# Kernel optimization log

Hardware: AMD Instinct MI355X
Metric: run time of the kernel (lower is better)

The kernel has to match this reference:

```python
import jax, jax.numpy as jnp
import numpy as np

N, IN_SIZE, FEAT, N_OUT = 8192, 512, 128, 512
ALPHA = 0.5


def setup_inputs() -> dict:
    key = jax.random.key(0)
    ks = jax.random.split(key, 5)
    return {
        "x": jax.random.normal(ks[0], (N, IN_SIZE), dtype=jnp.float32),
        "W0": jax.random.normal(ks[1], (FEAT, IN_SIZE), dtype=jnp.float32) * (1.0 / np.sqrt(IN_SIZE)),
        "W1": jax.random.normal(ks[2], (FEAT, IN_SIZE), dtype=jnp.float32) * (1.0 / np.sqrt(IN_SIZE)),
        "weight": jax.random.normal(ks[3], (IN_SIZE, N_OUT), dtype=jnp.float32),
        "weight_time": jax.random.normal(ks[4], (IN_SIZE, N_OUT), dtype=jnp.float32),
    }


def time_affinity(n: int) -> jnp.ndarray:
    # Closed form of the numpy roll/triu/flip construction: M[i,j] = n - |i-j|,
    # then rows normalized to sum to 1.
    idx = jnp.arange(n)
    M = (n - jnp.abs(idx[:, None] - idx[None, :])).astype(jnp.float32)
    return M / jnp.sum(M, axis=1, keepdims=True)


def reference(x, W0, W1, weight, weight_time):
    n = x.shape[0]
    q = x @ W0.T                      # [N, FEAT]
    k = x @ W1.T                      # [N, FEAT]
    G = jax.nn.softmax(q @ k.T, axis=1)   # [N, N] learned affinity
    G_time = time_affinity(n)              # [N, N] static affinity
    out = (G @ x) @ weight                 # [N, N_OUT]
    out_time = (G_time @ x) @ weight_time  # [N, N_OUT]
    return ALPHA * out + (1.0 - ALPHA) * out_time
```

## Files before the change

kernel.cpp:

```cpp
#include <hip/hip_runtime.h>
#include <math.h>

#define NN 8192
#define INS 512
#define FEAT 128

typedef unsigned short ush;
typedef short bf16x8 __attribute__((ext_vector_type(8)));
typedef float f32x4 __attribute__((ext_vector_type(4)));

__device__ __forceinline__ ush f2bf(float f) {
    unsigned u = __float_as_uint(f);
    unsigned r = (u + 0x7FFFu + ((u >> 16) & 1u)) >> 16;
    return (ush)r;
}
__device__ __forceinline__ float bf2f(ush h) {
    return __uint_as_float(((unsigned)h) << 16);
}
__device__ __forceinline__ void cp16(const ush* g, ush* l) {
    __builtin_amdgcn_global_load_lds(
        (const __attribute__((address_space(1))) void*)g,
        (__attribute__((address_space(3))) void*)l, 16, 0, 0);
}
__device__ __forceinline__ void split8(float4 f0, float4 f1, uint4& h, uint4& l) {
    float f[8] = {f0.x, f0.y, f0.z, f0.w, f1.x, f1.y, f1.z, f1.w};
    unsigned hu[8], lu[8];
    #pragma unroll
    for (int j = 0; j < 8; ++j) {
        unsigned u = __float_as_uint(f[j]);
        hu[j] = u >> 16;
        float lo = f[j] - __uint_as_float(u & 0xFFFF0000u);
        lu[j] = (unsigned)f2bf(lo);
    }
    h.x = hu[0] | (hu[1] << 16); h.y = hu[2] | (hu[3] << 16);
    h.z = hu[4] | (hu[5] << 16); h.w = hu[6] | (hu[7] << 16);
    l.x = lu[0] | (lu[1] << 16); l.y = lu[2] | (lu[3] << 16);
    l.z = lu[4] | (lu[5] << 16); l.w = lu[6] | (lu[7] << 16);
}


__global__ __launch_bounds__(256) void cast_w01(const float* __restrict__ W0,
                                                const float* __restrict__ W1,
                                                ush* __restrict__ W01h,
                                                ush* __restrict__ W01l) {
    int idx = (blockIdx.x * 256 + threadIdx.x) * 8;
    int r = idx >> 9, c = idx & 511;
    const float* src = (r < 128) ? &W0[r * 512 + c] : &W1[(r - 128) * 512 + c];
    float4 f0 = *(const float4*)src;
    float4 f1 = *(const float4*)(src + 4);
    uint4 h, l;
    split8(f0, f1, h, l);
    *(uint4*)&W01h[idx] = h;
    *(uint4*)&W01l[idx] = l;
}

__global__ __launch_bounds__(256) void cast_wT(const float* __restrict__ wm,
                                               const float* __restrict__ wt,
                                               ush* __restrict__ wmTh, ush* __restrict__ wmTl,
                                               ush* __restrict__ wtTh, ush* __restrict__ wtTl) {
    const float* src = blockIdx.z ? wt : wm;
    ush* oh = blockIdx.z ? wtTh : wmTh;
    ush* ol = blockIdx.z ? wtTl : wmTl;
    __shared__ float T[64][65];
    const int t = threadIdx.x;
    const int k0 = blockIdx.y * 64, n0 = blockIdx.x * 64;
    #pragma unroll
    for (int u = 0; u < 4; ++u) {
        int idx = u * 256 + t;
        int r = idx >> 4, c4 = (idx & 15) * 4;
        *(float4*)&T[r][c4] = *(const float4*)&src[(k0 + r) * 512 + n0 + c4];
    }
    __syncthreads();
    #pragma unroll
    for (int u = 0; u < 4; ++u) {
        int idx = u * 256 + t;
        int a = idx >> 4, b4 = (idx & 15) * 4;
        unsigned hu[4], lu[4];
        #pragma unroll
        for (int j = 0; j < 4; ++j) {
            float f = T[b4 + j][a];
            unsigned uu = __float_as_uint(f);
            hu[j] = uu >> 16;
            lu[j] = (unsigned)f2bf(f - __uint_as_float(uu & 0xFFFF0000u));
        }
        uint2 hp, lp;
        hp.x = hu[0] | (hu[1] << 16); hp.y = hu[2] | (hu[3] << 16);
        lp.x = lu[0] | (lu[1] << 16); lp.y = lu[2] | (lu[3] << 16);
        *(uint2*)&oh[(n0 + a) * 512 + k0 + b4] = hp;
        *(uint2*)&ol[(n0 + a) * 512 + k0 + b4] = lp;
    }
}

__global__ __launch_bounds__(256) void gemm_xv(const float* __restrict__ x,
    const ush* __restrict__ wmTh, const ush* __restrict__ wmTl,
    const ush* __restrict__ wtTh, const ush* __restrict__ wtTl,
    ush* __restrict__ vtg, ush* __restrict__ xtb) {
    const bool isV = (blockIdx.z == 0);
    const ush* Bhg = isV ? wmTh : wtTh;
    const ush* Blg = isV ? wmTl : wtTl;
    __shared__ __align__(16) ush sm[20480];
    ush* Ah = sm;
    ush* Al = sm + 5120;
    ush* Bh = sm + 10240;
    ush* Bl = sm + 15360;
    const int t = threadIdx.x;
    const int lane = t & 63, w = t >> 6;
    const int l15 = lane & 15, g4 = lane >> 4;
    const int m0 = blockIdx.y * 128, n0 = blockIdx.x * 128;
    const int wm0 = (w & 1) * 64, wn0 = (w >> 1) * 64;
    f32x4 acc[4][4];
    #pragma unroll
    for (int mt = 0; mt < 4; ++mt)
        #pragma unroll
        for (int nt = 0; nt < 4; ++nt)
            acc[mt][nt] = (f32x4){0.f, 0.f, 0.f, 0.f};

    const int am = t >> 1, akh = (t & 1) * 16;
    for (int k0 = 0; k0 < 512; k0 += 32) {
        __syncthreads();
        {
            const float* src = &x[(m0 + am) * 512 + k0 + akh];
            float4 f0 = *(const float4*)&src[0];
            float4 f1 = *(const float4*)&src[4];
            float4 f2 = *(const float4*)&src[8];
            float4 f3 = *(const float4*)&src[12];
            uint4 h0, l0, h1, l1;
            split8(f0, f1, h0, l0);
            split8(f2, f3, h1, l1);
            int s0 = am * 5 + (akh >> 3);
            *(uint4*)&Ah[s0 * 8] = h0; *(uint4*)&Ah[(s0 + 1) * 8] = h1;
            *(uint4*)&Al[s0 * 8] = l0; *(uint4*)&Al[(s0 + 1) * 8] = l1;
        }
        #pragma unroll
        for (int u = 0; u < 2; ++u) {
            int s = u * 256 + t;
            int n = s >> 2, g = s & 3;
            int srco = (n0 + n) * 512 + k0 + g * 8;
            int slot = n * 5 + g;
            *(uint4*)&Bh[slot * 8] = *(const uint4*)&Bhg[srco];
            *(uint4*)&Bl[slot * 8] = *(const uint4*)&Blg[srco];
        }
        __syncthreads();
        bf16x8 ah[4], al[4], bh[4], bl[4];
        #pragma unroll
        for (int mt = 0; mt < 4; ++mt) {
            int slot = (wm0 + mt * 16 + l15) * 5 + g4;
            ah[mt] = *(const bf16x8*)&Ah[slot * 8];
            al[mt] = *(const bf16x8*)&Al[slot * 8];
        }
        #pragma unroll
        for (int nt = 0; nt < 4; ++nt) {
            int slot = (wn0 + nt * 16 + l15) * 5 + g4;
            bh[nt] = *(const bf16x8*)&Bh[slot * 8];
            bl[nt] = *(const bf16x8*)&Bl[slot * 8];
        }
        #pragma unroll
        for (int mt = 0; mt < 4; ++mt)
            #pragma unroll
            for (int nt = 0; nt < 4; ++nt) {
                acc[mt][nt] = __builtin_amdgcn_mfma_f32_16x16x32_bf16(ah[mt], bh[nt], acc[mt][nt], 0, 0, 0);
                acc[mt][nt] = __builtin_amdgcn_mfma_f32_16x16x32_bf16(al[mt], bh[nt], acc[mt][nt], 0, 0, 0);
                acc[mt][nt] = __builtin_amdgcn_mfma_f32_16x16x32_bf16(ah[mt], bl[nt], acc[mt][nt], 0, 0, 0);
            }
    }

    if (!isV) {
        #pragma unroll
        for (int mt = 0; mt < 4; ++mt)
            #pragma unroll
            for (int nt = 0; nt < 4; ++nt) {
                int col = n0 + wn0 + nt * 16 + l15;
                int rowb = m0 + wm0 + mt * 16 + g4 * 4;
                #pragma unroll
                for (int reg = 0; reg < 4; ++reg)
                    xtb[(rowb + reg) * 512 + col] = f2bf(acc[mt][nt][reg]);
            }
    } else {
        __syncthreads();
        #pragma unroll
        for (int mt = 0; mt < 4; ++mt)
            #pragma unroll
            for (int nt = 0; nt < 4; ++nt) {
                int nl = wn0 + nt * 16 + l15;
                int mb = wm0 + mt * 16 + g4 * 4;
                uint2 pk;
                pk.x = (unsigned)f2bf(acc[mt][nt][0]) | ((unsigned)f2bf(acc[mt][nt][1]) << 16);
                pk.y = (unsigned)f2bf(acc[mt][nt][2]) | ((unsigned)f2bf(acc[mt][nt][3]) << 16);
                *(uint2*)&sm[nl * 136 + mb] = pk;
            }
        __syncthreads();
        int a = t >> 1, off = (t & 1) * 64;
        #pragma unroll
        for (int u = 0; u < 8; ++u)
            *(uint4*)&vtg[(n0 + a) * 8192 + m0 + off + u * 8] =
                *(const uint4*)&sm[a * 136 + off + u * 8];
    }
}

__global__ __launch_bounds__(256) void gemm_qk(const float* __restrict__ x,
    const ush* __restrict__ W01h, const ush* __restrict__ W01l,
    ush* __restrict__ qh, ush* __restrict__ ql,
    ush* __restrict__ kh, ush* __restrict__ kl) {
    __shared__ __align__(16) ush sm[15360];
    ush* Ah = sm;
    ush* Al = sm + 2560;
    ush* Bh = sm + 5120;
    ush* Bl = sm + 10240;
    const int t = threadIdx.x;
    const int lane = t & 63, w = t >> 6;
    const int l15 = lane & 15, g4 = lane >> 4;
    const int m0 = blockIdx.y * 64, n0 = blockIdx.x * 128;
    const int wm0 = (w & 1) * 32, wn0 = (w >> 1) * 64;
    f32x4 acc[2][4];
    #pragma unroll
    for (int mt = 0; mt < 2; ++mt)
        #pragma unroll
        for (int nt = 0; nt < 4; ++nt)
            acc[mt][nt] = (f32x4){0.f, 0.f, 0.f, 0.f};

    const int ar = t >> 2, ag = t & 3;
    for (int k0 = 0; k0 < 512; k0 += 32) {
        __syncthreads();
        {
            const float* src = &x[(m0 + ar) * 512 + k0 + ag * 8];
            float4 f0 = *(const float4*)&src[0];
            float4 f1 = *(const float4*)&src[4];
            uint4 h, l;
            split8(f0, f1, h, l);
            int slot = ar * 5 + ag;
            *(uint4*)&Ah[slot * 8] = h;
            *(uint4*)&Al[slot * 8] = l;
        }
        #pragma unroll
        for (int u = 0; u < 2; ++u) {
            int s = u * 256 + t;
            int n = s >> 2, g = s & 3;
            int srco = (n0 + n) * 512 + k0 + g * 8;
            int slot = n * 5 + g;
            *(uint4*)&Bh[slot * 8] = *(const uint4*)&W01h[srco];
            *(uint4*)&Bl[slot * 8] = *(const uint4*)&W01l[srco];
        }
        __syncthreads();
        bf16x8 ah[2], al[2], bh[4], bl[4];
        #pragma unroll
        for (int mt = 0; mt < 2; ++mt) {
            int slot = (wm0 + mt * 16 + l15) * 5 + g4;
            ah[mt] = *(const bf16x8*)&Ah[slot * 8];
            al[mt] = *(const bf16x8*)&Al[slot * 8];
        }
        #pragma unroll
        for (int nt = 0; nt < 4; ++nt) {
            int slot = (wn0 + nt * 16 + l15) * 5 + g4;
            bh[nt] = *(const bf16x8*)&Bh[slot * 8];
            bl[nt] = *(const bf16x8*)&Bl[slot * 8];
        }
        #pragma unroll
        for (int mt = 0; mt < 2; ++mt)
            #pragma unroll
            for (int nt = 0; nt < 4; ++nt) {
                acc[mt][nt] = __builtin_amdgcn_mfma_f32_16x16x32_bf16(ah[mt], bh[nt], acc[mt][nt], 0, 0, 0);
                acc[mt][nt] = __builtin_amdgcn_mfma_f32_16x16x32_bf16(al[mt], bh[nt], acc[mt][nt], 0, 0, 0);
                acc[mt][nt] = __builtin_amdgcn_mfma_f32_16x16x32_bf16(ah[mt], bl[nt], acc[mt][nt], 0, 0, 0);
            }
    }
    ush* oh = (n0 == 0) ? qh : kh;
    ush* ol = (n0 == 0) ? ql : kl;
    #pragma unroll
    for (int mt = 0; mt < 2; ++mt)
        #pragma unroll
        for (int nt = 0; nt < 4; ++nt) {
            int col = wn0 + nt * 16 + l15;
            int rowb = m0 + wm0 + mt * 16 + g4 * 4;
            #pragma unroll
            for (int reg = 0; reg < 4; ++reg) {
                float v = acc[mt][nt][reg];
                unsigned u = __float_as_uint(v);
                ush h = (ush)(u >> 16);
                ush lo = f2bf(v - __uint_as_float(u & 0xFFFF0000u));
                oh[(rowb + reg) * 128 + col] = h;
                ol[(rowb + reg) * 128 + col] = lo;
            }
        }
}

__global__ __launch_bounds__(256) void time_part1(const ush* __restrict__ xtb,
                                                  float* __restrict__ pP,
                                                  float* __restrict__ pQ) {
    int d = blockIdx.x * 256 + threadIdx.x;
    int r0 = blockIdx.y * 128;
    float sp = 0.f, sq = 0.f;
    for (int r = 0; r < 128; ++r) {
        float v = bf2f(xtb[(r0 + r) * 512 + d]);
        sp += v;
        sq += (float)(r0 + r) * v;
    }
    pP[blockIdx.y * 512 + d] = sp;
    pQ[blockIdx.y * 512 + d] = sq;
}

__global__ __launch_bounds__(512) void time_part2(float* __restrict__ pP,
                                                  float* __restrict__ pQ,
                                                  float* __restrict__ Ad,
                                                  float* __restrict__ Qt) {
    int d = threadIdx.x;
    float rp = 0.f, rq = 0.f;
    for (int c = 0; c < 64; ++c) {
        int idx = c * 512 + d;
        float p = pP[idx], qv = pQ[idx];
        pP[idx] = rp; pQ[idx] = rq;
        rp += p; rq += qv;
    }
    Ad[d] = rp; Qt[d] = rq;
}

__global__ __launch_bounds__(256) void time_part3(const ush* __restrict__ xtb,
                                                  const float* __restrict__ pP,
                                                  const float* __restrict__ pQ,
                                                  const float* __restrict__ Ad,
                                                  const float* __restrict__ Qt,
                                                  float* __restrict__ out) {
    int d = blockIdx.x * 256 + threadIdx.x;
    int r0 = blockIdx.y * 128;
    float P = pP[blockIdx.y * 512 + d];
    float Q = pQ[blockIdx.y * 512 + d];
    float A = Ad[d], Qtot = Qt[d];
    for (int r = 0; r < 128; ++r) {
        int i = r0 + r;
        float v = bf2f(xtb[i * 512 + d]);
        P += v;
        float fi = (float)i;
        Q += fi * v;
        float B = 2.f * fi * P - 2.f * Q + Qtot - fi * A;
        int Si = 67108864 - (i * (i + 1)) / 2 - ((8191 - i) * (8192 - i)) / 2;
        float T = (8192.f * A - B) / (float)Si;
        out[i * 512 + d] = 0.5f * T;
    }
}

__global__ __launch_bounds__(512, 2) void pass2(const ush* __restrict__ qhg,
                                                const ush* __restrict__ qlg,
                                                const ush* __restrict__ khg,
                                                const ush* __restrict__ klg,
                                                const ush* __restrict__ vtg,
                                                ush* __restrict__ part0,
                                                ush* __restrict__ part1,
                                                float* __restrict__ lh) {
    __shared__ __align__(16) ush Kh0[512 * 8],  Kh1[512 * 8];
    __shared__ __align__(16) ush Kl0[512 * 8],  Kl1[512 * 8];
    __shared__ __align__(16) ush Vt0[2048 * 8], Vt1[2048 * 8];
    __shared__ __align__(16) ush Pd0[64 * 40],  Pd1[64 * 40];
    __shared__ float Linv[64];

    const int t = threadIdx.x;
    const int lane = t & 63, w = t >> 6;
    const int l15 = lane & 15, g = lane >> 4;
    const int b = blockIdx.x;
    const int xcd = b & 7, lid = b >> 3;
    const int jhalf = xcd >> 2;
    const int strip = (xcd & 3) * 32 + lid;
    const int i0 = strip * 64;
    const int jbase = jhalf * 4096;
    const bool isS = (w < 4);
    const int wp = w & 3;
    const float SHIFT = 32.0f;

    bf16x8 Qh[4], Ql[4];
    float l_run[4];
    if (isS) {
        int qrow = i0 + wp * 16 + l15;
        #pragma unroll
        for (int kt = 0; kt < 4; ++kt) {
            Qh[kt] = *(const bf16x8*)&qhg[qrow * 128 + kt * 32 + g * 8];
            Ql[kt] = *(const bf16x8*)&qlg[qrow * 128 + kt * 32 + g * 8];
        }
        #pragma unroll
        for (int reg = 0; reg < 4; ++reg) l_run[reg] = 0.f;
    }

    f32x4 acc[8][4];
    #pragma unroll
    for (int mt = 0; mt < 8; ++mt)
        #pragma unroll
        for (int nt = 0; nt < 4; ++nt)
            acc[mt][nt] = (f32x4){0.f, 0.f, 0.f, 0.f};

    auto stageK = [&](ush* KhD, ush* KlD, int j0) {
        int n = t >> 4, gl = (t & 15) ^ (n & 15);
        int src = (j0 + n) * 128 + gl * 8;
        cp16(&khg[src], &KhD[t * 8]);
        cp16(&klg[src], &KlD[t * 8]);
    };
    auto stageV = [&](ush* VtD, int j0) {
        #pragma unroll
        for (int u = 0; u < 4; ++u) {
            int s = u * 512 + t;
            int c = s >> 2, gl = (s & 3) ^ ((c >> 1) & 3);
            cp16(&vtg[c * 8192 + j0 + gl * 8], &VtD[s * 8]);
        }
    };
    auto pvStep = [&](const ush* VtR, const ush* Pr) {
        bf16x8 Pb[4];
        #pragma unroll
        for (int nt = 0; nt < 4; ++nt)
            Pb[nt] = *(const bf16x8*)&Pr[(nt * 16 + l15) * 40 + g * 8];
        #pragma unroll
        for (int mt = 0; mt < 8; ++mt) {
            int c = wp * 128 + mt * 16 + l15;
            int slot = c * 4 + (g ^ ((c >> 1) & 3));
            bf16x8 vfr = *(const bf16x8*)&VtR[slot * 8];
            #pragma unroll
            for (int nt = 0; nt < 4; ++nt)
                acc[mt][nt] = __builtin_amdgcn_mfma_f32_16x16x32_bf16(vfr, Pb[nt], acc[mt][nt], 0, 0, 0);
        }
    };

    stageK(Kh0, Kl0, jbase);
    __syncthreads();

    for (int jt = 0; jt < 128; ++jt) {
        ush* KhC = (jt & 1) ? Kh1 : Kh0;
        ush* KlC = (jt & 1) ? Kl1 : Kl0;
        ush* KhN = (jt & 1) ? Kh0 : Kh1;
        ush* KlN = (jt & 1) ? Kl0 : Kl1;
        ush* VtW = (jt & 1) ? Vt1 : Vt0;
        ush* VtR = (jt & 1) ? Vt0 : Vt1;
        ush* Pw  = (jt & 1) ? Pd1 : Pd0;
        ush* Pr  = (jt & 1) ? Pd0 : Pd1;

        stageV(VtW, jbase + jt * 32);
        if (jt < 127) stageK(KhN, KlN, jbase + (jt + 1) * 32);

        if (isS) {
            #pragma unroll
            for (int kh = 0; kh < 2; ++kh) {
                bf16x8 kbh[4], kbl[4];
                int n = kh * 16 + l15;
                #pragma unroll
                for (int kt = 0; kt < 4; ++kt) {
                    int slot = n * 16 + ((kt * 4 + g) ^ (n & 15));
                    kbh[kt] = *(const bf16x8*)&KhC[slot * 8];
                    kbl[kt] = *(const bf16x8*)&KlC[slot * 8];
                }
                f32x4 sa = {0.f, 0.f, 0.f, 0.f};
                f32x4 sb = {0.f, 0.f, 0.f, 0.f};
                f32x4 sc = {0.f, 0.f, 0.f, 0.f};
                #pragma unroll
                for (int kt = 0; kt < 4; ++kt) sa = __builtin_amdgcn_mfma_f32_16x16x32_bf16(Qh[kt], kbh[kt], sa, 0, 0, 0);
                #pragma unroll
                for (int kt = 0; kt < 4; ++kt) sb = __builtin_amdgcn_mfma_f32_16x16x32_bf16(Ql[kt], kbh[kt], sb, 0, 0, 0);
                #pragma unroll
                for (int kt = 0; kt < 4; ++kt) sc = __builtin_amdgcn_mfma_f32_16x16x32_bf16(Qh[kt], kbl[kt], sc, 0, 0, 0);
                #pragma unroll
                for (int reg = 0; reg < 4; ++reg) {
                    float s = (sa[reg] + sb[reg]) + sc[reg];
                    float p = __expf(s - SHIFT);
                    Pw[(wp * 16 + g * 4 + reg) * 40 + kh * 16 + l15] = f2bf(p);
                    l_run[reg] += p;
                }
            }
        } else if (jt > 0) {
            pvStep(VtR, Pr);
        }
        __syncthreads();
    }

    if (isS) {
        #pragma unroll
        for (int reg = 0; reg < 4; ++reg) {
            float rs = l_run[reg];
            #pragma unroll
            for (int st = 1; st < 16; st <<= 1) rs += __shfl_xor(rs, st);
            int row = wp * 16 + g * 4 + reg;
            if (l15 == 0) {
                Linv[row] = 1.0f / rs;
                lh[jhalf * 8192 + i0 + row] = rs;
            }
        }
    }
    __syncthreads();
    if (!isS) {
        pvStep(Vt1, Pd1);
        float li[4];
        #pragma unroll
        for (int nt = 0; nt < 4; ++nt) li[nt] = Linv[nt * 16 + l15];
        ush* prt = (jhalf == 0) ? part0 : part1;
        #pragma unroll
        for (int mt = 0; mt < 8; ++mt)
            #pragma unroll
            for (int nt = 0; nt < 4; ++nt) {
                int qrow = i0 + nt * 16 + l15;
                int vcol = wp * 128 + mt * 16 + g * 4;
                uint2 pk;
                pk.x = (unsigned)f2bf(acc[mt][nt][0] * li[nt]) |
                       ((unsigned)f2bf(acc[mt][nt][1] * li[nt]) << 16);
                pk.y = (unsigned)f2bf(acc[mt][nt][2] * li[nt]) |
                       ((unsigned)f2bf(acc[mt][nt][3] * li[nt]) << 16);
                *(uint2*)&prt[qrow * 512 + vcol] = pk;
            }
    }
}

__global__ __launch_bounds__(256) void merge_k(const ush* __restrict__ p0,
                                               const ush* __restrict__ p1,
                                               const float* __restrict__ lh,
                                               float* __restrict__ out) {
    int base = (blockIdx.x * 256 + threadIdx.x) * 8;
    int row = base >> 9;
    float l0 = lh[row], l1 = lh[8192 + row];
    float z = 0.5f / (l0 + l1);
    float w0 = l0 * z, w1 = l1 * z;
    uint4 a = *(const uint4*)&p0[base];
    uint4 b = *(const uint4*)&p1[base];
    float4 o0 = *(float4*)&out[base];
    float4 o1 = *(float4*)&out[base + 4];
    unsigned av[4] = {a.x, a.y, a.z, a.w};
    unsigned bv[4] = {b.x, b.y, b.z, b.w};
    float r[8];
    #pragma unroll
    for (int i = 0; i < 4; ++i) {
        r[2 * i + 0] = w0 * bf2f((ush)(av[i] & 0xFFFF)) + w1 * bf2f((ush)(bv[i] & 0xFFFF));
        r[2 * i + 1] = w0 * bf2f((ush)(av[i] >> 16))    + w1 * bf2f((ush)(bv[i] >> 16));
    }
    o0.x += r[0]; o0.y += r[1]; o0.z += r[2]; o0.w += r[3];
    o1.x += r[4]; o1.y += r[5]; o1.z += r[6]; o1.w += r[7];
    *(float4*)&out[base] = o0;
    *(float4*)&out[base + 4] = o1;
}

extern "C" void kernel_launch(void* const* d_in, const int* in_sizes, int n_in,
                              void* d_out, int out_size, void* d_ws, size_t ws_size,
                              hipStream_t stream) {
    const float* x  = (const float*)d_in[0];
    const float* W0 = (const float*)d_in[1];
    const float* W1 = (const float*)d_in[2];
    const float* wm = (const float*)d_in[3];
    const float* wt = (const float*)d_in[4];
    float* out = (float*)d_out;
    float* ws  = (float*)d_ws;

    ush* vtg = (ush*)(ws + 0);
    ush* xtb  = (ush*)(ws + 2097152);
    float* lhp = ws + 2097152;
    ush* W01h = (ush*)(ws + 4194304);
    ush* W01l = (ush*)(ws + 4259840);
    ush* wmTh = (ush*)(ws + 4325376);
    ush* wmTl = (ush*)(ws + 4456448);
    ush* wtTh = (ush*)(ws + 4587520);
    ush* wtTl = (ush*)(ws + 4718592);
    ush* part0 = (ush*)(ws + 4194304);
    ush* part1 = (ush*)(ws + 6291456);
    ush* qh = (ush*)(ws + 8388608);
    ush* ql = (ush*)(ws + 8912896);
    ush* kh = (ush*)(ws + 9437184);
    ush* kl = (ush*)(ws + 9961472);
    float* pP = ws + 10485760;
    float* pQ = ws + 10518528;
    float* Ad = ws + 10551296;
    float* Qt = ws + 10551808;

    cast_w01   <<<dim3(64),       256, 0, stream>>>(W0, W1, W01h, W01l);
    cast_wT    <<<dim3(8, 8, 2),  256, 0, stream>>>(wm, wt, wmTh, wmTl, wtTh, wtTl);
    gemm_xv    <<<dim3(4, 64, 2), 256, 0, stream>>>(x, wmTh, wmTl, wtTh, wtTl, vtg, xtb);
    gemm_qk    <<<dim3(2, 128),   256, 0, stream>>>(x, W01h, W01l, qh, ql, kh, kl);
    time_part1 <<<dim3(2, 64),    256, 0, stream>>>(xtb, pP, pQ);
    time_part2 <<<dim3(1),        512, 0, stream>>>(pP, pQ, Ad, Qt);
    time_part3 <<<dim3(2, 64),    256, 0, stream>>>(xtb, pP, pQ, Ad, Qt, out);
    pass2      <<<dim3(256),      512, 0, stream>>>(qh, ql, kh, kl, vtg, part0, part1, lhp);
    merge_k    <<<dim3(2048),     256, 0, stream>>>(part0, part1, lhp, out);
}
```

Measured before the change: 315.7 us.

## Halve pass2 row strip to 32 rows, load V directly from global into registers

The attention pass2 kernel now processes 32-row query strips instead of 64, doubling the grid to 512 blocks. The four score waves split the work as 2 row-quads by 2 key halves, and their partial row sums are combined through shared memory. V fragments are now read straight from global memory into registers by the PV waves instead of being staged in LDS. This cuts LDS use and registers so more blocks fit per CU (launch bounds raised to 4), giving more parallelism on the many-CU device. In exchange, each block re-reads V from global/L2 with half the reuse, and the global loads are not prefetched into LDS.

After: 995.6 us. +215.4%, slower.

```diff
diff --git a/kernel.cpp b/kernel.cpp
--- a/kernel.cpp
+++ b/kernel.cpp
@@ -337,7 +337,7 @@
     }
 }
 
-__global__ __launch_bounds__(512, 2) void pass2(const ush* __restrict__ qhg,
+__global__ __launch_bounds__(512, 4) void pass2(const ush* __restrict__ qhg,
                                                 const ush* __restrict__ qlg,
                                                 const ush* __restrict__ khg,
                                                 const ush* __restrict__ klg,
@@ -345,11 +345,10 @@
                                                 ush* __restrict__ part0,
                                                 ush* __restrict__ part1,
                                                 float* __restrict__ lh) {
-    __shared__ __align__(16) ush Kh0[512 * 8],  Kh1[512 * 8];
-    __shared__ __align__(16) ush Kl0[512 * 8],  Kl1[512 * 8];
-    __shared__ __align__(16) ush Vt0[2048 * 8], Vt1[2048 * 8];
-    __shared__ __align__(16) ush Pd0[64 * 40],  Pd1[64 * 40];
-    __shared__ float Linv[64];
+    __shared__ __align__(16) ush Kh0[512 * 8], Kh1[512 * 8];
+    __shared__ __align__(16) ush Kl0[512 * 8], Kl1[512 * 8];
+    __shared__ __align__(16) ush Pd0[32 * 40], Pd1[32 * 40];
+    __shared__ float Lp[2][32];
 
     const int t = threadIdx.x;
     const int lane = t & 63, w = t >> 6;
@@ -357,17 +356,19 @@
     const int b = blockIdx.x;
     const int xcd = b & 7, lid = b >> 3;
     const int jhalf = xcd >> 2;
-    const int strip = (xcd & 3) * 32 + lid;
-    const int i0 = strip * 64;
+    const int strip = (xcd & 3) * 64 + lid;
+    const int i0 = strip * 32;
     const int jbase = jhalf * 4096;
     const bool isS = (w < 4);
+    const int rq = w & 1;
+    const int kh = (w >> 1) & 1;
     const int wp = w & 3;
     const float SHIFT = 32.0f;
 
     bf16x8 Qh[4], Ql[4];
     float l_run[4];
     if (isS) {
-        int qrow = i0 + wp * 16 + l15;
+        int qrow = i0 + rq * 16 + l15;
         #pragma unroll
         for (int kt = 0; kt < 4; ++kt) {
             Qh[kt] = *(const bf16x8*)&qhg[qrow * 128 + kt * 32 + g * 8];
@@ -377,12 +378,13 @@
         for (int reg = 0; reg < 4; ++reg) l_run[reg] = 0.f;
     }
 
-    f32x4 acc[8][4];
+    f32x4 acc[8][2];
     #pragma unroll
     for (int mt = 0; mt < 8; ++mt)
         #pragma unroll
-        for (int nt = 0; nt < 4; ++nt)
+        for (int nt = 0; nt < 2; ++nt)
             acc[mt][nt] = (f32x4){0.f, 0.f, 0.f, 0.f};
+    bf16x8 vf[8];
 
     auto stageK = [&](ush* KhD, ush* KlD, int j0) {
         int n = t >> 4, gl = (t & 15) ^ (n & 15);
@@ -390,28 +392,21 @@
         cp16(&khg[src], &KhD[t * 8]);
         cp16(&klg[src], &KlD[t * 8]);
     };
-    auto stageV = [&](ush* VtD, int j0) {
-        #pragma unroll
-        for (int u = 0; u < 4; ++u) {
-            int s = u * 512 + t;
-            int c = s >> 2, gl = (s & 3) ^ ((c >> 1) & 3);
-            cp16(&vtg[c * 8192 + j0 + gl * 8], &VtD[s * 8]);
-        }
+    auto loadV = [&](int j0) {
+        #pragma unroll
+        for (int mt = 0; mt < 8; ++mt)
+            vf[mt] = *(const bf16x8*)&vtg[(wp * 128 + mt * 16 + l15) * 8192 + j0 + g * 8];
     };
-    auto pvStep = [&](const ush* VtR, const ush* Pr) {
-        bf16x8 Pb[4];
-        #pragma unroll
-        for (int nt = 0; nt < 4; ++nt)
+    auto pvStep = [&](const ush* Pr) {
+        bf16x8 Pb[2];
+        #pragma unroll
+        for (int nt = 0; nt < 2; ++nt)
             Pb[nt] = *(const bf16x8*)&Pr[(nt * 16 + l15) * 40 + g * 8];
         #pragma unroll
-        for (int mt = 0; mt < 8; ++mt) {
-            int c = wp * 128 + mt * 16 + l15;
-            int slot = c * 4 + (g ^ ((c >> 1) & 3));
-            bf16x8 vfr = *(const bf16x8*)&VtR[slot * 8];
-            #pragma unroll
-            for (int nt = 0; nt < 4; ++nt)
-                acc[mt][nt] = __builtin_amdgcn_mfma_f32_16x16x32_bf16(vfr, Pb[nt], acc[mt][nt], 0, 0, 0);
-        }
+        for (int mt = 0; mt < 8; ++mt)
+            #pragma unroll
+            for (int nt = 0; nt < 2; ++nt)
+                acc[mt][nt] = __builtin_amdgcn_mfma_f32_16x16x32_bf16(vf[mt], Pb[nt], acc[mt][nt], 0, 0, 0);
     };
 
     stageK(Kh0, Kl0, jbase);
@@ -422,44 +417,39 @@
         ush* KlC = (jt & 1) ? Kl1 : Kl0;
         ush* KhN = (jt & 1) ? Kh0 : Kh1;
         ush* KlN = (jt & 1) ? Kl0 : Kl1;
-        ush* VtW = (jt & 1) ? Vt1 : Vt0;
-        ush* VtR = (jt & 1) ? Vt0 : Vt1;
         ush* Pw  = (jt & 1) ? Pd1 : Pd0;
         ush* Pr  = (jt & 1) ? Pd0 : Pd1;
 
-        stageV(VtW, jbase + jt * 32);
         if (jt < 127) stageK(KhN, KlN, jbase + (jt + 1) * 32);
 
         if (isS) {
-            #pragma unroll
-            for (int kh = 0; kh < 2; ++kh) {
-                bf16x8 kbh[4], kbl[4];
-                int n = kh * 16 + l15;
-                #pragma unroll
-                for (int kt = 0; kt < 4; ++kt) {
-                    int slot = n * 16 + ((kt * 4 + g) ^ (n & 15));
-                    kbh[kt] = *(const bf16x8*)&KhC[slot * 8];
-                    kbl[kt] = *(const bf16x8*)&KlC[slot * 8];
-                }
-                f32x4 sa = {0.f, 0.f, 0.f, 0.f};
-                f32x4 sb = {0.f, 0.f, 0.f, 0.f};
-                f32x4 sc = {0.f, 0.f, 0.f, 0.f};
-                #pragma unroll
-                for (int kt = 0; kt < 4; ++kt) sa = __builtin_amdgcn_mfma_f32_16x16x32_bf16(Qh[kt], kbh[kt], sa, 0, 0, 0);
-                #pragma unroll
-                for (int kt = 0; kt < 4; ++kt) sb = __builtin_amdgcn_mfma_f32_16x16x32_bf16(Ql[kt], kbh[kt], sb, 0, 0, 0);
-                #pragma unroll
-                for (int kt = 0; kt < 4; ++kt) sc = __builtin_amdgcn_mfma_f32_16x16x32_bf16(Qh[kt], kbl[kt], sc, 0, 0, 0);
-                #pragma unroll
-                for (int reg = 0; reg < 4; ++reg) {
-                    float s = (sa[reg] + sb[reg]) + sc[reg];
-                    float p = __expf(s - SHIFT);
-                    Pw[(wp * 16 + g * 4 + reg) * 40 + kh * 16 + l15] = f2bf(p);
-                    l_run[reg] += p;
-                }
-            }
-        } else if (jt > 0) {
-            pvStep(VtR, Pr);
+            bf16x8 kbh[4], kbl[4];
+            int n = kh * 16 + l15;
+            #pragma unroll
+            for (int kt = 0; kt < 4; ++kt) {
+                int slot = n * 16 + ((kt * 4 + g) ^ (n & 15));
+                kbh[kt] = *(const bf16x8*)&KhC[slot * 8];
+                kbl[kt] = *(const bf16x8*)&KlC[slot * 8];
+            }
+            f32x4 sa = {0.f, 0.f, 0.f, 0.f};
+            f32x4 sb = {0.f, 0.f, 0.f, 0.f};
+            f32x4 sc = {0.f, 0.f, 0.f, 0.f};
+            #pragma unroll
+            for (int kt = 0; kt < 4; ++kt) sa = __builtin_amdgcn_mfma_f32_16x16x32_bf16(Qh[kt], kbh[kt], sa, 0, 0, 0);
+            #pragma unroll
+            for (int kt = 0; kt < 4; ++kt) sb = __builtin_amdgcn_mfma_f32_16x16x32_bf16(Ql[kt], kbh[kt], sb, 0, 0, 0);
+            #pragma unroll
+            for (int kt = 0; kt < 4; ++kt) sc = __builtin_amdgcn_mfma_f32_16x16x32_bf16(Qh[kt], kbl[kt], sc, 0, 0, 0);
+            #pragma unroll
+            for (int reg = 0; reg < 4; ++reg) {
+                float s = (sa[reg] + sb[reg]) + sc[reg];
+                float p = __expf(s - SHIFT);
+                Pw[(rq * 16 + g * 4 + reg) * 40 + kh * 16 + l15] = f2bf(p);
+                l_run[reg] += p;
+            }
+        } else {
+            if (jt > 0) pvStep(Pr);
+            loadV(jbase + jt * 32);
         }
         __syncthreads();
     }
@@ -470,24 +460,33 @@
             float rs = l_run[reg];
             #pragma unroll
             for (int st = 1; st < 16; st <<= 1) rs += __shfl_xor(rs, st);
-            int row = wp * 16 + g * 4 + reg;
-            if (l15 == 0) {
-                Linv[row] = 1.0f / rs;
-                lh[jhalf * 8192 + i0 + row] = rs;
-            }
-        }
+            if (l15 == 0) Lp[kh][rq * 16 + g * 4 + reg] = rs;
+        }
+    } else {
+        pvStep(Pd1);
     }
     __syncthreads();
-    if (!isS) {
-        pvStep(Vt1, Pd1);
-        float li[4];
-        #pragma unroll
-        for (int nt = 0; nt < 4; ++nt) li[nt] = Linv[nt * 16 + l15];
+
+    if (isS) {
+        if (kh == 0 && l15 == 0) {
+            #pragma unroll
+            for (int reg = 0; reg < 4; ++reg) {
+                int row = rq * 16 + g * 4 + reg;
+                lh[jhalf * 8192 + i0 + row] = Lp[0][row] + Lp[1][row];
+            }
+        }
+    } else {
+        float li[2];
+        #pragma unroll
+        for (int nt = 0; nt < 2; ++nt) {
+            int row = nt * 16 + l15;
+            li[nt] = 1.0f / (Lp[0][row] + Lp[1][row]);
+        }
         ush* prt = (jhalf == 0) ? part0 : part1;
         #pragma unroll
         for (int mt = 0; mt < 8; ++mt)
             #pragma unroll
-            for (int nt = 0; nt < 4; ++nt) {
+            for (int nt = 0; nt < 2; ++nt) {
                 int qrow = i0 + nt * 16 + l15;
                 int vcol = wp * 128 + mt * 16 + g * 4;
                 uint2 pk;
@@ -565,6 +564,6 @@
     time_part1 <<<dim3(2, 64),    256, 0, stream>>>(xtb, pP, pQ);
     time_part2 <<<dim3(1),        512, 0, stream>>>(pP, pQ, Ad, Qt);
     time_part3 <<<dim3(2, 64),    256, 0, stream>>>(xtb, pP, pQ, Ad, Qt, out);
-    pass2      <<<dim3(256),      512, 0, stream>>>(qh, ql, kh, kl, vtg, part0, part1, lhp);
+    pass2      <<<dim3(512),      512, 0, stream>>>(qh, ql, kh, kl, vtg, part0, part1, lhp);
     merge_k    <<<dim3(2048),     256, 0, stream>>>(part0, part1, lhp, out);
 }
```

## Fuse both weight GEMMs in gemm_xv to share one split-x tile

Applied to the files above, without the earlier changes.

Each gemm_xv block now computes both x@weight and x@weight_time for a 128x64 output tile, so x is loaded and split into hi/lo bf16 once instead of twice. B tiles are staged into LDS with async global_load_lds using an XOR-swizzled layout in place of padded register copies. The kernel also declares launch_bounds with two blocks per CU. In exchange each block holds two accumulator sets, which raises register pressure, and the grid stays at the same 512 blocks, each doing the same amount of MFMA work as before.

Measured after the change: 312.5 us. Within noise of the previous version (-1.0%).

```diff
diff --git a/kernel.cpp b/kernel.cpp
--- a/kernel.cpp
+++ b/kernel.cpp
@@ -91,31 +91,30 @@
     }
 }
 
-__global__ __launch_bounds__(256) void gemm_xv(const float* __restrict__ x,
+__global__ __launch_bounds__(256, 2) void gemm_xv(const float* __restrict__ x,
     const ush* __restrict__ wmTh, const ush* __restrict__ wmTl,
     const ush* __restrict__ wtTh, const ush* __restrict__ wtTl,
     ush* __restrict__ vtg, ush* __restrict__ xtb) {
-    const bool isV = (blockIdx.z == 0);
-    const ush* Bhg = isV ? wmTh : wtTh;
-    const ush* Blg = isV ? wmTl : wtTl;
-    __shared__ __align__(16) ush sm[20480];
-    ush* Ah = sm;
-    ush* Al = sm + 5120;
-    ush* Bh = sm + 10240;
-    ush* Bl = sm + 15360;
+    __shared__ __align__(16) ush smA[10240];
+    __shared__ __align__(16) ush Bmh[2048], Bml[2048], Bth[2048], Btl[2048];
+    ush* Ah = smA;
+    ush* Al = smA + 5120;
     const int t = threadIdx.x;
     const int lane = t & 63, w = t >> 6;
     const int l15 = lane & 15, g4 = lane >> 4;
-    const int m0 = blockIdx.y * 128, n0 = blockIdx.x * 128;
-    const int wm0 = (w & 1) * 64, wn0 = (w >> 1) * 64;
-    f32x4 acc[4][4];
+    const int m0 = blockIdx.y * 128, n0 = blockIdx.x * 64;
+    const int wm0 = (w & 1) * 64, wn0 = (w >> 1) * 32;
+    f32x4 accm[4][2], acct[4][2];
     #pragma unroll
     for (int mt = 0; mt < 4; ++mt)
         #pragma unroll
-        for (int nt = 0; nt < 4; ++nt)
-            acc[mt][nt] = (f32x4){0.f, 0.f, 0.f, 0.f};
+        for (int nt = 0; nt < 2; ++nt) {
+            accm[mt][nt] = (f32x4){0.f, 0.f, 0.f, 0.f};
+            acct[mt][nt] = (f32x4){0.f, 0.f, 0.f, 0.f};
+        }
 
     const int am = t >> 1, akh = (t & 1) * 16;
+    const int bn = t >> 2, bg = (t & 3) ^ ((t >> 2) & 3);
     for (int k0 = 0; k0 < 512; k0 += 32) {
         __syncthreads();
         {
@@ -131,69 +130,73 @@
             *(uint4*)&Ah[s0 * 8] = h0; *(uint4*)&Ah[(s0 + 1) * 8] = h1;
             *(uint4*)&Al[s0 * 8] = l0; *(uint4*)&Al[(s0 + 1) * 8] = l1;
         }
-        #pragma unroll
-        for (int u = 0; u < 2; ++u) {
-            int s = u * 256 + t;
-            int n = s >> 2, g = s & 3;
-            int srco = (n0 + n) * 512 + k0 + g * 8;
-            int slot = n * 5 + g;
-            *(uint4*)&Bh[slot * 8] = *(const uint4*)&Bhg[srco];
-            *(uint4*)&Bl[slot * 8] = *(const uint4*)&Blg[srco];
+        {
+            int srco = (n0 + bn) * 512 + k0 + bg * 8;
+            cp16(&wmTh[srco], &Bmh[t * 8]);
+            cp16(&wmTl[srco], &Bml[t * 8]);
+            cp16(&wtTh[srco], &Bth[t * 8]);
+            cp16(&wtTl[srco], &Btl[t * 8]);
         }
         __syncthreads();
-        bf16x8 ah[4], al[4], bh[4], bl[4];
+        bf16x8 ah[4], al[4];
         #pragma unroll
         for (int mt = 0; mt < 4; ++mt) {
             int slot = (wm0 + mt * 16 + l15) * 5 + g4;
             ah[mt] = *(const bf16x8*)&Ah[slot * 8];
             al[mt] = *(const bf16x8*)&Al[slot * 8];
         }
-        #pragma unroll
-        for (int nt = 0; nt < 4; ++nt) {
-            int slot = (wn0 + nt * 16 + l15) * 5 + g4;
-            bh[nt] = *(const bf16x8*)&Bh[slot * 8];
-            bl[nt] = *(const bf16x8*)&Bl[slot * 8];
+        bf16x8 bmh[2], bml[2], bth[2], btl[2];
+        #pragma unroll
+        for (int nt = 0; nt < 2; ++nt) {
+            int n = wn0 + nt * 16 + l15;
+            int slot = n * 4 + (g4 ^ (n & 3));
+            bmh[nt] = *(const bf16x8*)&Bmh[slot * 8];
+            bml[nt] = *(const bf16x8*)&Bml[slot * 8];
+            bth[nt] = *(const bf16x8*)&Bth[slot * 8];
+            btl[nt] = *(const bf16x8*)&Btl[slot * 8];
         }
         #pragma unroll
         for (int mt = 0; mt < 4; ++mt)
             #pragma unroll
-            for (int nt = 0; nt < 4; ++nt) {
-                acc[mt][nt] = __builtin_amdgcn_mfma_f32_16x16x32_bf16(ah[mt], bh[nt], acc[mt][nt], 0, 0, 0);
-                acc[mt][nt] = __builtin_amdgcn_mfma_f32_16x16x32_bf16(al[mt], bh[nt], acc[mt][nt], 0, 0, 0);
-                acc[mt][nt] = __builtin_amdgcn_mfma_f32_16x16x32_bf16(ah[mt], bl[nt], acc[mt][nt], 0, 0, 0);
+            for (int nt = 0; nt < 2; ++nt) {
+                accm[mt][nt] = __builtin_amdgcn_mfma_f32_16x16x32_bf16(ah[mt], bmh[nt], accm[mt][nt], 0, 0, 0);
+                accm[mt][nt] = __builtin_amdgcn_mfma_f32_16x16x32_bf16(al[mt], bmh[nt], accm[mt][nt], 0, 0, 0);
+                accm[mt][nt] = __builtin_amdgcn_mfma_f32_16x16x32_bf16(ah[mt], bml[nt], accm[mt][nt], 0, 0, 0);
+                acct[mt][nt] = __builtin_amdgcn_mfma_f32_16x16x32_bf16(ah[mt], bth[nt], acct[mt][nt], 0, 0, 0);
+                acct[mt][nt] = __builtin_amdgcn_mfma_f32_16x16x32_bf16(al[mt], bth[nt], acct[mt][nt], 0, 0, 0);
+                acct[mt][nt] = __builtin_amdgcn_mfma_f32_16x16x32_bf16(ah[mt], btl[nt], acct[mt][nt], 0, 0, 0);
             }
     }
 
-    if (!isV) {
-        #pragma unroll
-        for (int mt = 0; mt < 4; ++mt)
-            #pragma unroll
-            for (int nt = 0; nt < 4; ++nt) {
-                int col = n0 + wn0 + nt * 16 + l15;
-                int rowb = m0 + wm0 + mt * 16 + g4 * 4;
-                #pragma unroll
-                for (int reg = 0; reg < 4; ++reg)
-                    xtb[(rowb + reg) * 512 + col] = f2bf(acc[mt][nt][reg]);
-            }
-    } else {
-        __syncthreads();
-        #pragma unroll
-        for (int mt = 0; mt < 4; ++mt)
-            #pragma unroll
-            for (int nt = 0; nt < 4; ++nt) {
-                int nl = wn0 + nt * 16 + l15;
-                int mb = wm0 + mt * 16 + g4 * 4;
-                uint2 pk;
-                pk.x = (unsigned)f2bf(acc[mt][nt][0]) | ((unsigned)f2bf(acc[mt][nt][1]) << 16);
-                pk.y = (unsigned)f2bf(acc[mt][nt][2]) | ((unsigned)f2bf(acc[mt][nt][3]) << 16);
-                *(uint2*)&sm[nl * 136 + mb] = pk;
-            }
-        __syncthreads();
-        int a = t >> 1, off = (t & 1) * 64;
-        #pragma unroll
-        for (int u = 0; u < 8; ++u)
+    #pragma unroll
+    for (int mt = 0; mt < 4; ++mt)
+        #pragma unroll
+        for (int nt = 0; nt < 2; ++nt) {
+            int col = n0 + wn0 + nt * 16 + l15;
+            int rowb = m0 + wm0 + mt * 16 + g4 * 4;
+            #pragma unroll
+            for (int reg = 0; reg < 4; ++reg)
+                xtb[(rowb + reg) * 512 + col] = f2bf(acct[mt][nt][reg]);
+        }
+    __syncthreads();
+    #pragma unroll
+    for (int mt = 0; mt < 4; ++mt)
+        #pragma unroll
+        for (int nt = 0; nt < 2; ++nt) {
+            int nl = wn0 + nt * 16 + l15;
+            int mb = wm0 + mt * 16 + g4 * 4;
+            uint2 pk;
+            pk.x = (unsigned)f2bf(accm[mt][nt][0]) | ((unsigned)f2bf(accm[mt][nt][1]) << 16);
+            pk.y = (unsigned)f2bf(accm[mt][nt][2]) | ((unsigned)f2bf(accm[mt][nt][3]) << 16);
+            *(uint2*)&smA[nl * 136 + mb] = pk;
+        }
+    __syncthreads();
+    {
+        int a = t >> 2, off = (t & 3) * 32;
+        #pragma unroll
+        for (int u = 0; u < 4; ++u)
             *(uint4*)&vtg[(n0 + a) * 8192 + m0 + off + u * 8] =
-                *(const uint4*)&sm[a * 136 + off + u * 8];
+                *(const uint4*)&smA[a * 136 + off + u * 8];
     }
 }
 
@@ -560,7 +563,7 @@
 
     cast_w01   <<<dim3(64),       256, 0, stream>>>(W0, W1, W01h, W01l);
     cast_wT    <<<dim3(8, 8, 2),  256, 0, stream>>>(wm, wt, wmTh, wmTl, wtTh, wtTl);
-    gemm_xv    <<<dim3(4, 64, 2), 256, 0, stream>>>(x, wmTh, wmTl, wtTh, wtTl, vtg, xtb);
+    gemm_xv    <<<dim3(8, 64),    256, 0, stream>>>(x, wmTh, wmTl, wtTh, wtTl, vtg, xtb);
     gemm_qk    <<<dim3(2, 128),   256, 0, stream>>>(x, W01h, W01l, qh, ql, kh, kl);
     time_part1 <<<dim3(2, 64),    256, 0, stream>>>(xtb, pP, pQ);
     time_part2 <<<dim3(1),        512, 0, stream>>>(pP, pQ, Ad, Qt);
```
